# Optimization experiments

Hardware: AMD Instinct MI355X
Metric: run time of the kernel (lower is better)

## Reference

```python
import jax, jax.numpy as jnp
import numpy as np

B, C_IN, H, W = 32, 128, 64, 64
C_OUT, KH, KW = 256, 3, 3


def setup_inputs() -> dict:
    key = jax.random.key(0)
    k1, k2, k3 = jax.random.split(key, 3)
    inputs = jax.random.normal(k1, (B, C_IN, H, W), dtype=jnp.float32)
    weights = jax.random.normal(k2, (C_OUT, C_IN, KH, KW), dtype=jnp.float32) * 0.05
    bias = jax.random.normal(k3, (C_OUT, 1), dtype=jnp.float32)
    return {"inputs": inputs, "weights": weights, "bias": bias}


def reference(inputs, weights, bias):
    # Direct 2D valid convolution, stride 1, padding 0 (module default).
    # output[b,o,i,j] = sum_{c,u,v} inputs[b,c,i+u,j+v] * weights[o,c,u,v] + bias[o]
    out = jax.lax.conv_general_dilated(
        inputs, weights,
        window_strides=(1, 1),
        padding="VALID",
        dimension_numbers=("NCHW", "OIHW", "NCHW"),
    )
    # bias has shape (C_out, 1); broadcast per output channel
    return out + bias.reshape(1, -1, 1, 1)
```

## Files before the change

kernel.cpp:

```cpp
#include <hip/hip_runtime.h>
#include <hip/hip_bf16.h>
#include <stdint.h>

#define BB   32
#define CIN  128
#define HH   64
#define WW   64
#define COUT 256
#define OHH  62
#define OWW  62
#define PIX_PER_B (OHH*OWW)
#define NPIX (BB*PIX_PER_B)
#define KTOT (9*CIN)
#define NKT  36
#define SLOT 24576

typedef __bf16 bf16x8 __attribute__((ext_vector_type(8)));
typedef float  f32x4  __attribute__((ext_vector_type(4)));
typedef uint16_t u16x8 __attribute__((ext_vector_type(8)));

__device__ __forceinline__ uint16_t f2bf(float f) {
    uint32_t u = __float_as_uint(f);
    uint32_t r = (u + 0x7FFFu + ((u >> 16) & 1u)) >> 16;
    return (uint16_t)r;
}

__device__ __forceinline__ void gload_lds16(const void* g, void* l) {
    __builtin_amdgcn_global_load_lds(
        (const __attribute__((address_space(1))) uint32_t*)g,
        (__attribute__((address_space(3))) uint32_t*)l, 16, 0, 0);
}

__global__ void __launch_bounds__(256) to_nhwc(const float* __restrict__ in,
                                               uint16_t* __restrict__ out) {
    int slab = blockIdx.x;
    int b = slab >> 6, h = slab & 63;
    int w  = threadIdx.x & 63;
    int cp = threadIdx.x >> 6;
    const float* src = in + (((size_t)b * CIN) * HH + h) * WW + w;
    uint16_t* dst = out + ((size_t)slab * WW + w) * CIN;
    #pragma unroll
    for (int it = 0; it < 4; ++it) {
        int c0 = cp * 32 + it * 8;
        u16x8 v;
        #pragma unroll
        for (int j = 0; j < 8; ++j) v[j] = f2bf(src[(c0 + j) * (HH * WW)]);
        *reinterpret_cast<u16x8*>(dst + c0) = v;
    }
}

__global__ void __launch_bounds__(256) pack_w(const float* __restrict__ w,
                                              uint16_t* __restrict__ out) {
    int idx = blockIdx.x * 256 + threadIdx.x;
    int o = idx / KTOT;
    int k = idx - o * KTOT;
    int uv = k >> 7, c = k & 127;
    out[idx] = f2bf(w[(o * CIN + c) * 9 + uv]);
}

__global__ void __launch_bounds__(512, 4) conv_k32(
        const uint16_t* __restrict__ Xg,
        const uint16_t* __restrict__ Wg,
        const float*    __restrict__ bias,
        float*          __restrict__ out)
{
    __shared__ char lds[3 * SLOT + 1024];
    int* pbase = (int*)(lds + 3 * SLOT);
    int* obase = pbase + 128;

    const int tid  = threadIdx.x;
    const int lane = tid & 63;
    const int wid  = tid >> 6;

    int bid = blockIdx.x;
    int xcd = bid & 7, lid = bid >> 3;
    int nt  = (xcd == 0 ? lid : 121 + (xcd - 1) * 120 + lid);

    if (tid < 128) {
        int n   = nt * 128 + tid;
        int b   = n / PIX_PER_B;
        int rem = n - b * PIX_PER_B;
        int oh  = rem / OWW;
        int ow  = rem - oh * OWW;
        pbase[tid] = ((b * 64 + oh) * 64 + ow) * 128;
        obase[tid] = b * (COUT * PIX_PER_B) + rem;
    }
    __syncthreads();

    const int cs   = (((tid & 3) ^ ((tid >> 3) & 3)) << 4);
    const int ldst = tid * 16;
    const char* WgB = (const char*)Wg;
    const char* XgB = (const char*)Xg;
    const int aow0 = (tid >> 2) * (KTOT * 2);
    const int aow1 = (128 + (tid >> 2)) * (KTOT * 2);
    const int pxw  = pbase[tid >> 2] * 2;

    const int wm = wid >> 1, wn = wid & 1;
    int aro[4], xro[4];
    #pragma unroll
    for (int mi = 0; mi < 4; ++mi) {
        int row = wm * 64 + mi * 16 + (lane & 15);
        aro[mi] = row * 64 + ((((lane >> 4) ^ ((row >> 1) & 3))) << 4);
    }
    #pragma unroll
    for (int nj = 0; nj < 4; ++nj) {
        int row = wn * 64 + nj * 16 + (lane & 15);
        xro[nj] = 16384 + row * 64 + ((((lane >> 4) ^ ((row >> 1) & 3))) << 4);
    }

    f32x4 acc[4][4] = {};

    auto stage = [&](int t, char* dst) {
        int uvv = t >> 2;
        int u   = (uvv * 11) >> 5;
        int v   = uvv - u * 3;
        int kb  = ((t & 3) << 6) + cs;
        gload_lds16(WgB + aow0 + uvv * 256 + kb, dst + ldst);
        gload_lds16(WgB + aow1 + uvv * 256 + kb, dst + 8192 + ldst);
        gload_lds16(XgB + pxw + (u * 64 + v) * 256 + kb, dst + 16384 + ldst);
    };

    stage(0, lds);
    stage(1, lds + SLOT);
    asm volatile("s_waitcnt vmcnt(3)" ::: "memory");
    __builtin_amdgcn_s_barrier();

    int s = 0, s2 = 2;
    for (int t = 0; t < NKT; ++t) {
        char* slot = lds + s * SLOT;
        bf16x8 af[4], xf[4];
        #pragma unroll
        for (int mi = 0; mi < 4; ++mi)
            af[mi] = *reinterpret_cast<const bf16x8*>(slot + aro[mi]);
        #pragma unroll
        for (int nj = 0; nj < 4; ++nj)
            xf[nj] = *reinterpret_cast<const bf16x8*>(slot + xro[nj]);
        if (t + 2 < NKT) stage(t + 2, lds + s2 * SLOT);
        __builtin_amdgcn_s_barrier();
        asm volatile("s_waitcnt lgkmcnt(0)" ::: "memory");
        __builtin_amdgcn_sched_barrier(0);
        __builtin_amdgcn_s_setprio(1);
        #pragma unroll
        for (int mi = 0; mi < 4; ++mi)
            #pragma unroll
            for (int nj = 0; nj < 4; ++nj)
                acc[mi][nj] = __builtin_amdgcn_mfma_f32_16x16x32_bf16(
                    af[mi], xf[nj], acc[mi][nj], 0, 0, 0);
        __builtin_amdgcn_s_setprio(0);
        if (t < NKT - 2)
            asm volatile("s_waitcnt vmcnt(3)" ::: "memory");
        else if (t == NKT - 2)
            asm volatile("s_waitcnt vmcnt(0)" ::: "memory");
        __builtin_amdgcn_s_barrier();
        s  = (s  == 2) ? 0 : s  + 1;
        s2 = (s2 == 2) ? 0 : s2 + 1;
    }

    #pragma unroll
    for (int mi = 0; mi < 4; ++mi) {
        int o = wm * 64 + mi * 16 + ((lane >> 4) << 2);
        #pragma unroll
        for (int reg = 0; reg < 4; ++reg) {
            float bv = bias[o + reg];
            #pragma unroll
            for (int nj = 0; nj < 4; ++nj) {
                int pl = wn * 64 + nj * 16 + (lane & 15);
                out[obase[pl] + (o + reg) * PIX_PER_B] = acc[mi][nj][reg] + bv;
            }
        }
    }
}

__global__ void __launch_bounds__(256) conv_naive(const float* __restrict__ in,
                                                  const float* __restrict__ w,
                                                  const float* __restrict__ bias,
                                                  float* __restrict__ out) {
    long idx = (long)blockIdx.x * 256 + threadIdx.x;
    int t = (int)idx;
    int ow = t % OWW; t /= OWW;
    int oh = t % OHH; t /= OHH;
    int o  = t % COUT;
    int b  = t / COUT;
    float s = bias[o];
    for (int c = 0; c < CIN; ++c)
        for (int u = 0; u < 3; ++u)
            for (int v = 0; v < 3; ++v)
                s += in[((b * CIN + c) * HH + oh + u) * WW + ow + v] *
                     w[((o * CIN + c) * 3 + u) * 3 + v];
    out[idx] = s;
}

extern "C" void kernel_launch(void* const* d_in, const int* in_sizes, int n_in,
                              void* d_out, int out_size, void* d_ws, size_t ws_size,
                              hipStream_t stream) {
    const float* in   = (const float*)d_in[0];
    const float* wt   = (const float*)d_in[1];
    const float* bias = (const float*)d_in[2];
    float* out = (float*)d_out;

    const size_t xg_elems = (size_t)BB * HH * WW * CIN;
    const size_t wg_elems = (size_t)COUT * KTOT;
    const size_t need = (xg_elems + wg_elems) * sizeof(uint16_t);

    if (ws_size < need) {
        long total = (long)BB * COUT * OHH * OWW;
        conv_naive<<<(int)((total + 255) / 256), 256, 0, stream>>>(in, wt, bias, out);
        return;
    }

    uint16_t* Xg = (uint16_t*)d_ws;
    uint16_t* Wg = Xg + xg_elems;

    to_nhwc<<<BB * HH, 256, 0, stream>>>(in, Xg);
    pack_w<<<(COUT * KTOT) / 256, 256, 0, stream>>>(wt, Wg);
    conv_k32<<<NPIX / 128, 512, 0, stream>>>(Xg, Wg, bias, out);
}
```

Baseline: 109.6 us.

## Unroll conv main loop by three and drop the mid-iteration barrier

The K loop is manually unrolled by the three LDS slots, so slot offsets become compile-time constants. The global-to-LDS prefetch for step t+2 is now issued before the fragment reads, and the per-step address math is simplified with precomputed base pointers. The second barrier, the explicit lgkmcnt wait, the sched_barrier and the setprio calls are removed, leaving one barrier per step. This reduces synchronisation and scalar overhead and gives the compiler freedom to interleave LDS reads with MFMAs, at the cost of larger code and less explicit control over scheduling.

After: 112.4 us. +2.6%, slower.

```diff
diff --git a/kernel.cpp b/kernel.cpp
--- a/kernel.cpp
+++ b/kernel.cpp
@@ -89,11 +89,9 @@
 
     const int cs   = (((tid & 3) ^ ((tid >> 3) & 3)) << 4);
     const int ldst = tid * 16;
-    const char* WgB = (const char*)Wg;
-    const char* XgB = (const char*)Xg;
-    const int aow0 = (tid >> 2) * (KTOT * 2);
-    const int aow1 = (128 + (tid >> 2)) * (KTOT * 2);
-    const int pxw  = pbase[tid >> 2] * 2;
+    const char* aptr0 = (const char*)Wg + (tid >> 2) * (KTOT * 2) + cs;
+    const char* aptr1 = (const char*)Wg + (128 + (tid >> 2)) * (KTOT * 2) + cs;
+    const char* xptr  = (const char*)Xg + pbase[tid >> 2] * 2 + cs;
 
     const int wm = wid >> 1, wn = wid & 1;
     int aro[4], xro[4];
@@ -114,47 +112,44 @@
         int uvv = t >> 2;
         int u   = (uvv * 11) >> 5;
         int v   = uvv - u * 3;
-        int kb  = ((t & 3) << 6) + cs;
-        gload_lds16(WgB + aow0 + uvv * 256 + kb, dst + ldst);
-        gload_lds16(WgB + aow1 + uvv * 256 + kb, dst + 8192 + ldst);
-        gload_lds16(XgB + pxw + (u * 64 + v) * 256 + kb, dst + 16384 + ldst);
+        int xo  = (u << 14) | (v << 8) | ((t & 3) << 6);
+        gload_lds16(aptr0 + t * 64, dst + ldst);
+        gload_lds16(aptr1 + t * 64, dst + 8192 + ldst);
+        gload_lds16(xptr + xo, dst + 16384 + ldst);
     };
+
+#define PHASE(T, S, S2, STG, VMC, BAR) do {                                    \
+    char* _slot = lds + (S) * SLOT;                                            \
+    if (STG) stage((T) + 2, lds + (S2) * SLOT);                                \
+    bf16x8 af[4], xf[4];                                                       \
+    _Pragma("unroll") for (int mi = 0; mi < 4; ++mi)                           \
+        af[mi] = *reinterpret_cast<const bf16x8*>(_slot + aro[mi]);            \
+    _Pragma("unroll") for (int nj = 0; nj < 4; ++nj)                           \
+        xf[nj] = *reinterpret_cast<const bf16x8*>(_slot + xro[nj]);            \
+    _Pragma("unroll") for (int mi = 0; mi < 4; ++mi)                           \
+      _Pragma("unroll") for (int nj = 0; nj < 4; ++nj)                         \
+        acc[mi][nj] = __builtin_amdgcn_mfma_f32_16x16x32_bf16(                 \
+            af[mi], xf[nj], acc[mi][nj], 0, 0, 0);                             \
+    if ((VMC) == 1) asm volatile("s_waitcnt vmcnt(3)" ::: "memory");           \
+    else if ((VMC) == 2) asm volatile("s_waitcnt vmcnt(0)" ::: "memory");      \
+    if (BAR) __builtin_amdgcn_s_barrier();                                     \
+} while (0)
 
     stage(0, lds);
     stage(1, lds + SLOT);
     asm volatile("s_waitcnt vmcnt(3)" ::: "memory");
     __builtin_amdgcn_s_barrier();
 
-    int s = 0, s2 = 2;
-    for (int t = 0; t < NKT; ++t) {
-        char* slot = lds + s * SLOT;
-        bf16x8 af[4], xf[4];
-        #pragma unroll
-        for (int mi = 0; mi < 4; ++mi)
-            af[mi] = *reinterpret_cast<const bf16x8*>(slot + aro[mi]);
-        #pragma unroll
-        for (int nj = 0; nj < 4; ++nj)
-            xf[nj] = *reinterpret_cast<const bf16x8*>(slot + xro[nj]);
-        if (t + 2 < NKT) stage(t + 2, lds + s2 * SLOT);
-        __builtin_amdgcn_s_barrier();
-        asm volatile("s_waitcnt lgkmcnt(0)" ::: "memory");
-        __builtin_amdgcn_sched_barrier(0);
-        __builtin_amdgcn_s_setprio(1);
-        #pragma unroll
-        for (int mi = 0; mi < 4; ++mi)
-            #pragma unroll
-            for (int nj = 0; nj < 4; ++nj)
-                acc[mi][nj] = __builtin_amdgcn_mfma_f32_16x16x32_bf16(
-                    af[mi], xf[nj], acc[mi][nj], 0, 0, 0);
-        __builtin_amdgcn_s_setprio(0);
-        if (t < NKT - 2)
-            asm volatile("s_waitcnt vmcnt(3)" ::: "memory");
-        else if (t == NKT - 2)
-            asm volatile("s_waitcnt vmcnt(0)" ::: "memory");
-        __builtin_amdgcn_s_barrier();
-        s  = (s  == 2) ? 0 : s  + 1;
-        s2 = (s2 == 2) ? 0 : s2 + 1;
-    }
+    for (int i = 0; i < 11; ++i) {
+        const int t = 3 * i;
+        PHASE(t + 0, 0, 2, 1, 1, 1);
+        PHASE(t + 1, 1, 0, 1, 1, 1);
+        PHASE(t + 2, 2, 1, 1, 1, 1);
+    }
+    PHASE(33, 0, 2, 1, 1, 1);
+    PHASE(34, 1, 0, 0, 2, 1);
+    PHASE(35, 2, 1, 0, 0, 0);
+#undef PHASE
 
     #pragma unroll
     for (int mi = 0; mi < 4; ++mi) {
```
